# Kernel tuning notes

Measured on AMD Instinct MI355X. Metric: run time of the kernel, lower is better.

The kernel has to match this reference:

```python
import jax, jax.numpy as jnp
import numpy as np

B, IN_DIM, OUT_DIM, N, H = 64, 2, 1, 512, 64
SEQ, HOR, K, NSUP = 12, 12, 2, 2
TOT = 1 + NSUP * K  # number of diffusion matrices (identity + K steps per support)


def _lin_init(key, fan_in, shape):
    return jax.random.normal(key, shape, jnp.float32) / np.sqrt(fan_in)


def setup_inputs() -> dict:
    key = jax.random.key(0)
    ks = jax.random.split(key, 16)
    inputs = jax.random.normal(ks[0], (B, IN_DIM, N, SEQ), jnp.float32)
    A = jax.random.uniform(ks[1], (NSUP, N, N), jnp.float32)
    supports = A / A.sum(axis=2, keepdims=True)  # row-normalized transition matrices
    params = {}
    i = 2
    for pre, in0 in (('e', IN_DIM), ('d', OUT_DIM)):
        for l in range(2):
            cin = (in0 if l == 0 else H) + H
            params[f'{pre}{l}_wg'] = _lin_init(ks[i], TOT * cin, (TOT * cin, 2 * H)); i += 1
            params[f'{pre}{l}_bg'] = jnp.zeros((2 * H,), jnp.float32)
            params[f'{pre}{l}_wc'] = _lin_init(ks[i], TOT * cin, (TOT * cin, H)); i += 1
            params[f'{pre}{l}_bc'] = jnp.zeros((H,), jnp.float32)
    params['proj_w'] = _lin_init(ks[i], H, (OUT_DIM, H))
    params['proj_b'] = jnp.zeros((OUT_DIM,), jnp.float32)
    return {'inputs': inputs, 'supports': supports, **params}


def _gconv(x, h, supports, W, b):
    # x: (B,Cx,N), h: (B,H,N) -> (B,Dout,N)
    z = jnp.concatenate([x, h], axis=1)
    feats = [z]
    for s in range(NSUP):
        xk = z
        for _ in range(K):
            xk = jnp.einsum('nm,bcm->bcn', supports[s], xk)
            feats.append(xk)
    zf = jnp.concatenate(feats, axis=1)  # (B, TOT*C, N)
    return jnp.einsum('bcn,cd->bdn', zf, W) + b[None, :, None]


def _cell(x, h, supports, wg, bg, wc, bc):
    ru = jax.nn.sigmoid(_gconv(x, h, supports, wg, bg))
    r, u = jnp.split(ru, 2, axis=1)
    c = jnp.tanh(_gconv(x, r * h, supports, wc, bc))
    return u * h + (1.0 - u) * c


def _run(inputs, supports, p):
    h0 = jnp.zeros((B, H, N), jnp.float32)
    h1 = jnp.zeros((B, H, N), jnp.float32)

    def enc_step(carry, x):
        h0, h1 = carry
        h0 = _cell(x, h0, supports, p['e0_wg'], p['e0_bg'], p['e0_wc'], p['e0_bc'])
        h1 = _cell(h0, h1, supports, p['e1_wg'], p['e1_bg'], p['e1_wc'], p['e1_bc'])
        return (h0, h1), None

    xs = jnp.moveaxis(inputs, -1, 0)  # (SEQ,B,IN_DIM,N)
    (h0, h1), _ = jax.lax.scan(enc_step, (h0, h1), xs)

    go = jnp.zeros((B, OUT_DIM, N), jnp.float32)

    def dec_step(carry, _):
        x, h0, h1 = carry
        h0 = _cell(x, h0, supports, p['d0_wg'], p['d0_bg'], p['d0_wc'], p['d0_bc'])
        h1 = _cell(h0, h1, supports, p['d1_wg'], p['d1_bg'], p['d1_wc'], p['d1_bc'])
        y = jnp.einsum('bhn,oh->bon', h1, p['proj_w']) + p['proj_b'][None, :, None]
        return (y, h0, h1), y

    _, ys = jax.lax.scan(dec_step, (go, h0, h1), None, length=HOR)
    return jnp.moveaxis(ys, 0, -1)  # (B, OUT_DIM, N, HOR)


def reference(inputs, supports, e0_wg, e0_bg, e0_wc, e0_bc, e1_wg, e1_bg, e1_wc, e1_bc,
              d0_wg, d0_bg, d0_wc, d0_bc, d1_wg, d1_bg, d1_wc, d1_bc, proj_w, proj_b):
    p = dict(e0_wg=e0_wg, e0_bg=e0_bg, e0_wc=e0_wc, e0_bc=e0_bc,
             e1_wg=e1_wg, e1_bg=e1_bg, e1_wc=e1_wc, e1_bc=e1_bc,
             d0_wg=d0_wg, d0_bg=d0_bg, d0_wc=d0_wc, d0_bc=d0_bc,
             d1_wg=d1_wg, d1_bg=d1_bg, d1_wc=d1_wc, d1_bc=d1_bc,
             proj_w=proj_w, proj_b=proj_b)
    return _run(inputs, supports, p)
```

## Files before the change

### kernel.cpp

```cpp
#include <hip/hip_runtime.h>

#define B_ 64
#define N_ 512

typedef __attribute__((ext_vector_type(8))) short bf8_t;
typedef __attribute__((ext_vector_type(16))) float f16_t;
typedef __attribute__((ext_vector_type(4))) float f4v_t;

#define MFMA32(a, b, c) __builtin_amdgcn_mfma_f32_32x32x16_bf16(a, b, c, 0, 0, 0)

__device__ __forceinline__ ushort f2bf(float x) {
  union { float f; unsigned u; } v; v.f = x;
  unsigned r = v.u + 0x7FFFu + ((v.u >> 16) & 1u);
  return (ushort)(r >> 16);
}
__device__ __forceinline__ float bf2f(ushort h) {
  union { unsigned u; float f; } v; v.u = ((unsigned)h) << 16;
  return v.f;
}

__device__ __forceinline__ void gld16(const ushort* g, ushort* l) {
  __builtin_amdgcn_global_load_lds(
      (const __attribute__((address_space(1))) unsigned int*)(uintptr_t)g,
      (__attribute__((address_space(3))) unsigned int*)(uintptr_t)l,
      16, 0, 0);
}

__device__ __forceinline__ int xcd_logical(int nwg) {
  int lin = blockIdx.x + gridDim.x * (blockIdx.y + gridDim.y * blockIdx.z);
  return (lin & 7) * (nwg >> 3) + (lin >> 3);
}

__device__ __forceinline__ int swz32(int r) { return (r >> 1) & 3; }

template <int ROWS, int THREADS>
__device__ __forceinline__ void stage_tile2(const ushort* g, int lda, int k0,
                                            ushort* l, int tid) {
  constexpr int RT = (ROWS * 32) / (THREADS * 8);
#pragma unroll
  for (int q = 0; q < RT; ++q) {
    int e  = q * THREADS * 8 + tid * 8;
    int r  = e >> 5;
    int c8 = (e >> 3) & 3;
    int g8 = c8 ^ swz32(r);
    gld16(g + (size_t)r * lda + k0 + g8 * 8, l + e);
  }
}

__device__ __forceinline__ int crow32(int r, int hb) {
  return (r & 3) + 8 * (r >> 2) + 4 * hb;
}

__device__ __forceinline__ void core128(
    const ushort* Ah, const ushort* Al, int lda,
    const ushort* Bh, const ushort* Bl, int ldb,
    int K, ushort* lds, f16_t acc[2][2]) {
  constexpr int TILE = 128 * 32;
  constexpr int SSZ  = 4 * TILE;
  const int tid = threadIdx.x, lane = tid & 63, wave = tid >> 6;
  const int ar = lane & 31, hb = lane >> 5;
  const int wm = wave >> 1, wn = wave & 1;

  auto stage = [&](int buf, int k0) {
    ushort* lb = lds + buf * SSZ;
    stage_tile2<128, 256>(Ah, lda, k0, lb, tid);
    stage_tile2<128, 256>(Al, lda, k0, lb + TILE, tid);
    stage_tile2<128, 256>(Bh, ldb, k0, lb + 2 * TILE, tid);
    stage_tile2<128, 256>(Bl, ldb, k0, lb + 3 * TILE, tid);
  };

  const int nc = K >> 5;
  stage(0, 0);
  int buf = 0;
  for (int c = 0; c < nc; ++c) {
    __syncthreads();
    if (c + 1 < nc) stage(buf ^ 1, (c + 1) << 5);
    const ushort* lb = lds + buf * SSZ;
#pragma unroll
    for (int ks = 0; ks < 2; ++ks) {
      bf8_t ah[2], al[2], bh[2], bl[2];
#pragma unroll
      for (int i = 0; i < 2; ++i) {
        int r = wm * 64 + 32 * i + ar;
        int c8 = (ks * 2 + hb) ^ swz32(r);
        ah[i] = *(const bf8_t*)(lb + r * 32 + c8 * 8);
        al[i] = *(const bf8_t*)(lb + TILE + r * 32 + c8 * 8);
      }
#pragma unroll
      for (int j = 0; j < 2; ++j) {
        int r = wn * 64 + 32 * j + ar;
        int c8 = (ks * 2 + hb) ^ swz32(r);
        bh[j] = *(const bf8_t*)(lb + 2 * TILE + r * 32 + c8 * 8);
        bl[j] = *(const bf8_t*)(lb + 3 * TILE + r * 32 + c8 * 8);
      }
#pragma unroll
      for (int i = 0; i < 2; ++i)
#pragma unroll
        for (int j = 0; j < 2; ++j) {
          acc[i][j] = MFMA32(ah[i], bh[j], acc[i][j]);
          acc[i][j] = MFMA32(ah[i], bl[j], acc[i][j]);
          acc[i][j] = MFMA32(al[i], bh[j], acc[i][j]);
        }
    }
    buf ^= 1;
  }
}

__device__ __forceinline__ void core128_1(
    const ushort* Ah, int lda,
    const ushort* Bh, int ldb,
    int K, ushort* lds, f16_t acc[2][2]) {
  constexpr int TILE = 128 * 32;
  constexpr int SSZ  = 2 * TILE;
  const int tid = threadIdx.x, lane = tid & 63, wave = tid >> 6;
  const int ar = lane & 31, hb = lane >> 5;
  const int wm = wave >> 1, wn = wave & 1;

  auto stage = [&](int buf, int k0) {
    ushort* lb = lds + buf * SSZ;
    stage_tile2<128, 256>(Ah, lda, k0, lb, tid);
    stage_tile2<128, 256>(Bh, ldb, k0, lb + TILE, tid);
  };

  const int nc = K >> 5;
  stage(0, 0);
  int buf = 0;
  for (int c = 0; c < nc; ++c) {
    __syncthreads();
    if (c + 1 < nc) stage(buf ^ 1, (c + 1) << 5);
    const ushort* lb = lds + buf * SSZ;
#pragma unroll
    for (int ks = 0; ks < 2; ++ks) {
      bf8_t ah[2], bh[2];
#pragma unroll
      for (int i = 0; i < 2; ++i) {
        int r = wm * 64 + 32 * i + ar;
        int c8 = (ks * 2 + hb) ^ swz32(r);
        ah[i] = *(const bf8_t*)(lb + r * 32 + c8 * 8);
      }
#pragma unroll
      for (int j = 0; j < 2; ++j) {
        int r = wn * 64 + 32 * j + ar;
        int c8 = (ks * 2 + hb) ^ swz32(r);
        bh[j] = *(const bf8_t*)(lb + TILE + r * 32 + c8 * 8);
      }
#pragma unroll
      for (int i = 0; i < 2; ++i)
#pragma unroll
        for (int j = 0; j < 2; ++j)
          acc[i][j] = MFMA32(ah[i], bh[j], acc[i][j]);
    }
    buf ^= 1;
  }
}

__global__ __launch_bounds__(256) void stb_k(const float* __restrict__ S,
                                             ushort* __restrict__ Bcat,
                                             ushort* __restrict__ STb) {
  __shared__ float tile[16][17];
  int s = blockIdx.z;
  int n0 = blockIdx.y * 16, m0 = blockIdx.x * 16;
  int tx = threadIdx.x & 15, ty = threadIdx.x >> 4;
  float v = S[(size_t)s * 262144 + (size_t)(n0 + ty) * 512 + m0 + tx];
  tile[ty][tx] = v;
  Bcat[(size_t)(n0 + ty) * 2048 + (size_t)(2 * s) * 512 + m0 + tx] = f2bf(v);
  __syncthreads();
  STb[(size_t)s * 262144 + (size_t)(m0 + ty) * 512 + n0 + tx] = f2bf(tile[tx][ty]);
}

__global__ __launch_bounds__(256) void ssqm_k(const ushort* __restrict__ Bc,
                                              const ushort* __restrict__ STb,
                                              ushort* __restrict__ Bout) {
  __shared__ __attribute__((aligned(16))) ushort lds[2 * 2 * 128 * 32];
  int tid = threadIdx.x, lane = tid & 63, wave = tid >> 6;
  int wm = wave >> 1, wn = wave & 1, ar = lane & 31, hb = lane >> 5;
  int a = blockIdx.x, bm = blockIdx.y, s = blockIdx.z;
  f16_t acc[2][2] = {};
  core128_1(Bc + (size_t)(a * 128) * 2048 + (size_t)(2 * s) * 512, 2048,
            STb + (size_t)s * 262144 + (size_t)(bm * 128) * 512, 512,
            512, lds, acc);
#pragma unroll
  for (int i = 0; i < 2; ++i)
#pragma unroll
    for (int j = 0; j < 2; ++j) {
      int m_ = bm * 128 + wn * 64 + 32 * j + ar;
#pragma unroll
      for (int r = 0; r < 16; ++r) {
        int n_ = a * 128 + wm * 64 + 32 * i + crow32(r, hb);
        Bout[(size_t)n_ * 2048 + (size_t)(2 * s + 1) * 512 + m_] = f2bf(acc[i][j][r]);
      }
    }
}

struct WSrc { const float* wg[4]; const float* wc[4]; };

__global__ __launch_bounds__(256) void wprep_all_k(WSrc src,
                                                   ushort* __restrict__ Wbuf) {
  int idx = blockIdx.x * 256 + threadIdx.x;
  if (idx >= 4 * 147456) return;
  int ci = idx / 147456, r = idx % 147456;
  int C = (ci == 0) ? 66 : (ci == 2) ? 65 : 128;
  const float* WG = src.wg[ci];
  const float* WC = src.wc[ci];
  ushort v;
  if (r < 32768) {
    int e = r & 16383, c = e & 127, d = e >> 7;
    float x = (c < C) ? WG[(size_t)c * 128 + d] : 0.f;
    ushort hh = f2bf(x);
    v = (r < 16384) ? hh : f2bf(x - bf2f(hh));
  } else if (r < 98304) {
    int e = r - 32768, c = e & 127, i = e >> 7;
    int t = 1 + (i >> 7), d = i & 127;
    v = (c < C) ? f2bf(WG[(size_t)(t * C + c) * 128 + d]) : (ushort)0;
  } else if (r < 114688) {
    int e = (r - 98304) & 8191, c = e & 127, d = e >> 7;
    float x = (c < C) ? WC[(size_t)c * 64 + d] : 0.f;
    ushort hh = f2bf(x);
    v = (r < 106496) ? hh : f2bf(x - bf2f(hh));
  } else {
    int e = r - 114688, c = e & 127, i = e >> 7;
    int t = 1 + (i >> 6), d = i & 63;
    v = (c < C) ? f2bf(WC[(size_t)(t * C + c) * 64 + d]) : (ushort)0;
  }
  Wbuf[idx] = v;
}

__global__ __launch_bounds__(256) void packzT_k(const float* __restrict__ xsrc,
                                                int xmode, int t, int Cx, int C,
                                                const float* __restrict__ hT,
                                                ushort* __restrict__ Zh,
                                                ushort* __restrict__ Zl) {
  int jg = blockIdx.x * 256 + threadIdx.x;
  int b = jg >> 9, n = jg & 511;
  for (int c0 = 0; c0 < 128; c0 += 8) {
    bf8_t vh, vl;
#pragma unroll
    for (int q = 0; q < 8; ++q) {
      int c = c0 + q;
      float v;
      if (c < Cx) {
        if (xmode == 0)      v = xsrc[((size_t)(b * Cx + c) * 512 + n) * 12 + t];
        else if (xmode == 1) v = xsrc[jg];
        else                 v = xsrc[(size_t)jg * 64 + c];
      } else if (c < C) {
        v = hT[(size_t)jg * 64 + (c - Cx)];
      } else {
        v = 0.f;
      }
      ushort hh = f2bf(v);
      vh[q] = (short)hh;
      vl[q] = (short)f2bf(v - bf2f(hh));
    }
    *(bf8_t*)(Zh + (size_t)jg * 128 + c0) = vh;
    *(bf8_t*)(Zl + (size_t)jg * 128 + c0) = vl;
  }
}

template <int MODE>
__global__ __launch_bounds__(256, 2) void g1_k(const ushort* __restrict__ Wih,
                                               const ushort* __restrict__ Wil,
                                               const ushort* __restrict__ Wd,
                                               const ushort* __restrict__ Zh,
                                               const ushort* __restrict__ Zl,
                                               ushort* __restrict__ Gh,
                                               float* __restrict__ G0T, int K) {
  __shared__ __attribute__((aligned(16))) ushort lds[2 * 4 * 128 * 32];
  constexpr int DR = (MODE == 0) ? 128 : 64;
  constexpr int NMT = (MODE == 0) ? 4 : 2;
  int tid = threadIdx.x, lane = tid & 63, wave = tid >> 6;
  int wm = wave >> 1, wn = wave & 1, ar = lane & 31, hb = lane >> 5;
  int L = xcd_logical(256 * (NMT + 1));
  int mt = L % (NMT + 1), nt = L / (NMT + 1);
  f16_t acc[2][2] = {};
  if (mt == NMT) {
    core128(Wih, Wil, 128,
            Zh + (size_t)nt * 128 * 128, Zl + (size_t)nt * 128 * 128, 128,
            K, lds, acc);
#pragma unroll
    for (int i = 0; i < 2; ++i)
#pragma unroll
      for (int j = 0; j < 2; ++j) {
        int jg = nt * 128 + wn * 64 + 32 * j + ar;
#pragma unroll
        for (int r = 0; r < 16; ++r) {
          int d = wm * 64 + 32 * i + crow32(r, hb);
          if (d >= DR) continue;
          G0T[(size_t)jg * DR + d] = acc[i][j][r];
        }
      }
  } else {
    core128_1(Wd + (size_t)mt * 128 * 128, 128,
              Zh + (size_t)nt * 128 * 128, 128,
              K, lds, acc);
#pragma unroll
    for (int i = 0; i < 2; ++i)
#pragma unroll
      for (int j = 0; j < 2; ++j) {
        int jg = nt * 128 + wn * 64 + 32 * j + ar;
        int b = jg >> 9, m = jg & 511;
#pragma unroll
        for (int r = 0; r < 16; ++r) {
          int ii = mt * 128 + wm * 64 + 32 * i + crow32(r, hb);
          int tt = ii / DR, d = ii % DR;
          Gh[((size_t)(b * DR + d)) * 2048 + (size_t)tt * 512 + m] = f2bf(acc[i][j][r]);
        }
      }
  }
}

__global__ __launch_bounds__(256, 3) void ru1g_k(const ushort* __restrict__ Gh,
                                                 const ushort* __restrict__ Bch,
                                                 float* __restrict__ P) {
  __shared__ __attribute__((aligned(16))) ushort lds[2 * 2 * 128 * 32];
  int tid = threadIdx.x, lane = tid & 63, wave = tid >> 6;
  int wm = wave >> 1, wn = wave & 1, ar = lane & 31, hb = lane >> 5;
  int L = xcd_logical(768);
  int mt = L & 3, nt = (L >> 2) & 63, kz = L >> 8;
  int k0 = kz * 768;
  int K  = (kz == 2) ? 512 : 768;
  f16_t acc[2][2] = {};
  core128_1(Bch + (size_t)mt * 128 * 2048 + k0, 2048,
            Gh + (size_t)nt * 128 * 2048 + k0, 2048,
            K, lds, acc);
  float* Pz = P + (size_t)kz * 4194304;
#pragma unroll
  for (int i = 0; i < 2; ++i)
#pragma unroll
    for (int j = 0; j < 2; ++j) {
      int R = nt * 128 + wn * 64 + 32 * j + ar;
      int b = R >> 7, d = R & 127;
#pragma unroll
      for (int r = 0; r < 16; ++r) {
        int node = mt * 128 + wm * 64 + 32 * i + crow32(r, hb);
        Pz[((size_t)b * 512 + node) * 128 + d] = acc[i][j][r];
      }
    }
}

__global__ __launch_bounds__(256) void ru1f_k(const float* __restrict__ P,
                                              const float* __restrict__ G0T,
                                              const float* __restrict__ bg,
                                              const float* __restrict__ hT,
                                              float* __restrict__ U,
                                              ushort* __restrict__ Zh,
                                              ushort* __restrict__ Zl, int Cx) {
  int i4 = blockIdx.x * 256 + threadIdx.x;
  if (i4 >= 1048576) return;
  int base = i4 * 4;
  int row = base >> 7, d = base & 127;
  f4v_t p0 = *(const f4v_t*)(P + base);
  f4v_t p1 = *(const f4v_t*)(P + 4194304 + base);
  f4v_t p2 = *(const f4v_t*)(P + 2 * 4194304 + base);
  f4v_t g0 = *(const f4v_t*)(G0T + base);
  if (d < 64) {
    f4v_t hv = *(const f4v_t*)(hT + (size_t)row * 64 + d);
#pragma unroll
    for (int e = 0; e < 4; ++e) {
      float s = 1.f / (1.f + expf(-(p0[e] + p1[e] + p2[e] + g0[e] + bg[d + e])));
      float rh = s * hv[e];
      ushort hh = f2bf(rh);
      Zh[(size_t)row * 128 + Cx + d + e] = hh;
      Zl[(size_t)row * 128 + Cx + d + e] = f2bf(rh - bf2f(hh));
    }
  } else {
    f4v_t uo;
#pragma unroll
    for (int e = 0; e < 4; ++e)
      uo[e] = 1.f / (1.f + expf(-(p0[e] + p1[e] + p2[e] + g0[e] + bg[d + e])));
    *(f4v_t*)(U + (size_t)row * 64 + (d - 64)) = uo;
  }
}

__global__ __launch_bounds__(256, 3) void ru2g_k(const ushort* __restrict__ Gh,
                                                 const ushort* __restrict__ Bch,
                                                 float* __restrict__ P) {
  __shared__ __attribute__((aligned(16))) ushort lds[2 * 2 * 128 * 32];
  int tid = threadIdx.x, lane = tid & 63, wave = tid >> 6;
  int wm = wave >> 1, wn = wave & 1, ar = lane & 31, hb = lane >> 5;
  int L = xcd_logical(512);
  int mt = L & 3, nt = (L >> 2) & 31, kz = L >> 7;
  f16_t acc[2][2] = {};
  core128_1(Bch + (size_t)mt * 128 * 2048 + kz * 512, 2048,
            Gh + (size_t)nt * 128 * 2048 + kz * 512, 2048,
            512, lds, acc);
  float* Pz = P + (size_t)kz * 2097152;
#pragma unroll
  for (int i = 0; i < 2; ++i)
#pragma unroll
    for (int j = 0; j < 2; ++j) {
      int R = nt * 128 + wn * 64 + 32 * j + ar;
      int b = R >> 6, d = R & 63;
#pragma unroll
      for (int r = 0; r < 16; ++r) {
        int node = mt * 128 + wm * 64 + 32 * i + crow32(r, hb);
        Pz[((size_t)b * 512 + node) * 64 + d] = acc[i][j][r];
      }
    }
}

__global__ __launch_bounds__(256) void ru2f_k(const float* __restrict__ P,
                                              const float* __restrict__ G0c,
                                              const float* __restrict__ bc,
                                              const float* __restrict__ U,
                                              float* __restrict__ hT) {
  int i4 = blockIdx.x * 256 + threadIdx.x;
  if (i4 >= 524288) return;
  int base = i4 * 4;
  int d = base & 63;
  f4v_t p0 = *(const f4v_t*)(P + base);
  f4v_t p1 = *(const f4v_t*)(P + 2097152 + base);
  f4v_t p2 = *(const f4v_t*)(P + 2 * 2097152 + base);
  f4v_t p3 = *(const f4v_t*)(P + 3 * 2097152 + base);
  f4v_t g0 = *(const f4v_t*)(G0c + base);
  f4v_t uv = *(const f4v_t*)(U + base);
  f4v_t hv = *(const f4v_t*)(hT + base);
#pragma unroll
  for (int e = 0; e < 4; ++e) {
    float ct = tanhf(p0[e] + p1[e] + p2[e] + p3[e] + g0[e] + bc[d + e]);
    hv[e] = uv[e] * hv[e] + (1.f - uv[e]) * ct;
  }
  *(f4v_t*)(hT + base) = hv;
}

__global__ __launch_bounds__(256) void proj_out_k(const float* __restrict__ h1T,
                                                  const float* __restrict__ pw,
                                                  const float* __restrict__ pb,
                                                  float* __restrict__ ybuf,
                                                  float* __restrict__ out, int k) {
  int idx = blockIdx.x * blockDim.x + threadIdx.x;
  if (idx >= B_ * N_) return;
  float s = pb[0];
  const float* hrow = h1T + (size_t)idx * 64;
#pragma unroll
  for (int j = 0; j < 64; ++j)
    s = fmaf(pw[j], hrow[j], s);
  ybuf[idx] = s;
  out[(size_t)idx * 12 + k] = s;
}

extern "C" void kernel_launch(void* const* d_in, const int* in_sizes, int n_in,
                              void* d_out, int out_size, void* d_ws, size_t ws_size,
                              hipStream_t stream) {
  const float* inputs   = (const float*)d_in[0];
  const float* supports = (const float*)d_in[1];
  WSrc wsrc;
  wsrc.wg[0] = (const float*)d_in[2];  wsrc.wg[1] = (const float*)d_in[6];
  wsrc.wg[2] = (const float*)d_in[10]; wsrc.wg[3] = (const float*)d_in[14];
  wsrc.wc[0] = (const float*)d_in[4];  wsrc.wc[1] = (const float*)d_in[8];
  wsrc.wc[2] = (const float*)d_in[12]; wsrc.wc[3] = (const float*)d_in[16];
  const float* Bg[4] = { (const float*)d_in[3],  (const float*)d_in[7],
                         (const float*)d_in[11], (const float*)d_in[15] };
  const float* Bc[4] = { (const float*)d_in[5],  (const float*)d_in[9],
                         (const float*)d_in[13], (const float*)d_in[17] };
  const float* proj_w = (const float*)d_in[18];
  const float* proj_b = (const float*)d_in[19];
  float* out = (float*)d_out;

  char* p = (char*)d_ws;
  auto carve = [&](size_t bytes) { void* q = p; p += (bytes + 255) & ~(size_t)255; return q; };
  ushort* Bch  = (ushort*)carve((size_t)512 * 2048 * 2);
  ushort* zTh  = (ushort*)carve((size_t)32768 * 128 * 2);
  ushort* zTl  = (ushort*)carve((size_t)32768 * 128 * 2);
  ushort* Gh   = (ushort*)carve((size_t)8192 * 2048 * 2);
  float*  G0T  = (float*)carve((size_t)32768 * 128 * 4);
  float*  P    = (float*)carve((size_t)3 * 4194304 * 4);
  float*  U    = (float*)carve((size_t)2097152 * 4);
  float*  h0   = (float*)carve((size_t)2097152 * 4);
  float*  h1   = (float*)carve((size_t)2097152 * 4);
  float*  ybuf = (float*)carve((size_t)B_ * N_ * 4);
  ushort* Wbuf = (ushort*)carve((size_t)4 * 147456 * 2);
  ushort* STb  = (ushort*)U;

  hipMemsetAsync(h0, 0, (size_t)2097152 * 4 * 2 + (size_t)B_ * N_ * 4, stream);

  stb_k<<<dim3(32, 32, 2), 256, 0, stream>>>(supports, Bch, STb);
  ssqm_k<<<dim3(4, 4, 2), 256, 0, stream>>>(Bch, STb, Bch);
  wprep_all_k<<<(4 * 147456 + 255) / 256, 256, 0, stream>>>(wsrc, Wbuf);

  auto cell = [&](int ci, int Cx, const float* x, int xmode, int t, float* h) {
    int C = Cx + 64;
    int K1 = (C + 31) & ~31;
    ushort* cw = Wbuf + (size_t)ci * 147456;
    ushort* Wgid_h = cw;          ushort* Wgid_l = cw + 16384;
    ushort* Wgd    = cw + 32768;
    ushort* Wcid_h = cw + 98304;  ushort* Wcid_l = cw + 106496;
    ushort* Wcd    = cw + 114688;
    packzT_k<<<128, 256, 0, stream>>>(x, xmode, t, Cx, C, h, zTh, zTl);
    g1_k<0><<<dim3(256, 5), 256, 0, stream>>>(Wgid_h, Wgid_l, Wgd, zTh, zTl, Gh, G0T, K1);
    ru1g_k<<<dim3(64, 4, 3), 256, 0, stream>>>(Gh, Bch, P);
    ru1f_k<<<4096, 256, 0, stream>>>(P, G0T, Bg[ci], h, U, zTh, zTl, Cx);
    g1_k<1><<<dim3(256, 3), 256, 0, stream>>>(Wcid_h, Wcid_l, Wcd, zTh, zTl, Gh, G0T, K1);
    ru2g_k<<<dim3(32, 4, 4), 256, 0, stream>>>(Gh, Bch, P);
    ru2f_k<<<2048, 256, 0, stream>>>(P, G0T, Bc[ci], U, h);
  };

  for (int t = 0; t < 12; ++t) {
    cell(0, 2, inputs, 0, t, h0);
    cell(1, 64, h0, 2, 0, h1);
  }
  for (int k = 0; k < 12; ++k) {
    cell(2, 1, ybuf, 1, 0, h0);
    cell(3, 64, h0, 2, 0, h1);
    proj_out_k<<<(B_ * N_ + 255) / 256, 256, 0, stream>>>(h1, proj_w, proj_b, ybuf, out, k);
  }
}
```

Measured before the change: 6.229 ms.

## Fuse Z-buffer packing into epilogues and shrink layer-0 K to 96

Drops the per-cell packzT_k kernel. ru2f_k and proj_out_k now write the bf16 hi/lo split of the new hidden state straight into persistent per-layer Z buffers, so layer 1's input comes from layer 0's epilogue and the decoder feedback from the projection. Layer-0 cells get their own 96-wide Z buffer, so the first GEMM uses K=96 instead of 128. Only the raw inputs are still packed each encoder step, plus a one-time transpose at the encoder/decoder switch. The cost is extra scalar bf16 stores in the elementwise epilogues, and correctness now depends on the zero-initialised padding columns staying valid.

```diff
diff --git a/kernel.cpp b/kernel.cpp
--- a/kernel.cpp
+++ b/kernel.cpp
@@ -225,35 +225,30 @@
   Wbuf[idx] = v;
 }
 
-__global__ __launch_bounds__(256) void packzT_k(const float* __restrict__ xsrc,
-                                                int xmode, int t, int Cx, int C,
-                                                const float* __restrict__ hT,
-                                                ushort* __restrict__ Zh,
-                                                ushort* __restrict__ Zl) {
+__global__ __launch_bounds__(256) void packx_k(const float* __restrict__ xsrc,
+                                               int t, ushort* __restrict__ Zh,
+                                               ushort* __restrict__ Zl) {
   int jg = blockIdx.x * 256 + threadIdx.x;
   int b = jg >> 9, n = jg & 511;
-  for (int c0 = 0; c0 < 128; c0 += 8) {
-    bf8_t vh, vl;
-#pragma unroll
-    for (int q = 0; q < 8; ++q) {
-      int c = c0 + q;
-      float v;
-      if (c < Cx) {
-        if (xmode == 0)      v = xsrc[((size_t)(b * Cx + c) * 512 + n) * 12 + t];
-        else if (xmode == 1) v = xsrc[jg];
-        else                 v = xsrc[(size_t)jg * 64 + c];
-      } else if (c < C) {
-        v = hT[(size_t)jg * 64 + (c - Cx)];
-      } else {
-        v = 0.f;
-      }
-      ushort hh = f2bf(v);
-      vh[q] = (short)hh;
-      vl[q] = (short)f2bf(v - bf2f(hh));
-    }
-    *(bf8_t*)(Zh + (size_t)jg * 128 + c0) = vh;
-    *(bf8_t*)(Zl + (size_t)jg * 128 + c0) = vl;
-  }
+#pragma unroll
+  for (int c = 0; c < 2; ++c) {
+    float v = xsrc[((size_t)(b * 2 + c) * 512 + n) * 12 + t];
+    ushort hh = f2bf(v);
+    Zh[(size_t)jg * 96 + c] = hh;
+    Zl[(size_t)jg * 96 + c] = f2bf(v - bf2f(hh));
+  }
+}
+
+__global__ __launch_bounds__(256) void trans_k(const float* __restrict__ hT0,
+                                               ushort* __restrict__ Zh,
+                                               ushort* __restrict__ Zl) {
+  int idx = blockIdx.x * 256 + threadIdx.x;
+  if (idx >= 32768 * 96) return;
+  int col = idx % 96, row = idx / 96;
+  float v = (col >= 1 && col <= 64) ? hT0[(size_t)row * 64 + (col - 1)] : 0.f;
+  ushort hh = f2bf(v);
+  Zh[(size_t)row * 96 + col] = hh;
+  Zl[(size_t)row * 96 + col] = f2bf(v - bf2f(hh));
 }
 
 template <int MODE>
@@ -263,7 +258,8 @@
                                                const ushort* __restrict__ Zh,
                                                const ushort* __restrict__ Zl,
                                                ushort* __restrict__ Gh,
-                                               float* __restrict__ G0T, int K) {
+                                               float* __restrict__ G0T,
+                                               int K, int zs) {
   __shared__ __attribute__((aligned(16))) ushort lds[2 * 4 * 128 * 32];
   constexpr int DR = (MODE == 0) ? 128 : 64;
   constexpr int NMT = (MODE == 0) ? 4 : 2;
@@ -274,7 +270,7 @@
   f16_t acc[2][2] = {};
   if (mt == NMT) {
     core128(Wih, Wil, 128,
-            Zh + (size_t)nt * 128 * 128, Zl + (size_t)nt * 128 * 128, 128,
+            Zh + (size_t)nt * 128 * zs, Zl + (size_t)nt * 128 * zs, zs,
             K, lds, acc);
 #pragma unroll
     for (int i = 0; i < 2; ++i)
@@ -290,7 +286,7 @@
       }
   } else {
     core128_1(Wd + (size_t)mt * 128 * 128, 128,
-              Zh + (size_t)nt * 128 * 128, 128,
+              Zh + (size_t)nt * 128 * zs, zs,
               K, lds, acc);
 #pragma unroll
     for (int i = 0; i < 2; ++i)
@@ -343,7 +339,8 @@
                                               const float* __restrict__ hT,
                                               float* __restrict__ U,
                                               ushort* __restrict__ Zh,
-                                              ushort* __restrict__ Zl, int Cx) {
+                                              ushort* __restrict__ Zl,
+                                              int cx, int zs) {
   int i4 = blockIdx.x * 256 + threadIdx.x;
   if (i4 >= 1048576) return;
   int base = i4 * 4;
@@ -359,8 +356,8 @@
       float s = 1.f / (1.f + expf(-(p0[e] + p1[e] + p2[e] + g0[e] + bg[d + e])));
       float rh = s * hv[e];
       ushort hh = f2bf(rh);
-      Zh[(size_t)row * 128 + Cx + d + e] = hh;
-      Zl[(size_t)row * 128 + Cx + d + e] = f2bf(rh - bf2f(hh));
+      Zh[(size_t)row * zs + cx + d + e] = hh;
+      Zl[(size_t)row * zs + cx + d + e] = f2bf(rh - bf2f(hh));
     }
   } else {
     f4v_t uo;
@@ -402,11 +399,16 @@
                                               const float* __restrict__ G0c,
                                               const float* __restrict__ bc,
                                               const float* __restrict__ U,
-                                              float* __restrict__ hT) {
+                                              float* __restrict__ hT,
+                                              ushort* __restrict__ Zsh,
+                                              ushort* __restrict__ Zsl,
+                                              int sx, int zs,
+                                              ushort* __restrict__ Z1h,
+                                              ushort* __restrict__ Z1l) {
   int i4 = blockIdx.x * 256 + threadIdx.x;
   if (i4 >= 524288) return;
   int base = i4 * 4;
-  int d = base & 63;
+  int row = base >> 6, d = base & 63;
   f4v_t p0 = *(const f4v_t*)(P + base);
   f4v_t p1 = *(const f4v_t*)(P + 2097152 + base);
   f4v_t p2 = *(const f4v_t*)(P + 2 * 2097152 + base);
@@ -418,6 +420,14 @@
   for (int e = 0; e < 4; ++e) {
     float ct = tanhf(p0[e] + p1[e] + p2[e] + p3[e] + g0[e] + bc[d + e]);
     hv[e] = uv[e] * hv[e] + (1.f - uv[e]) * ct;
+    ushort hh = f2bf(hv[e]);
+    ushort ll = f2bf(hv[e] - bf2f(hh));
+    Zsh[(size_t)row * zs + sx + d + e] = hh;
+    Zsl[(size_t)row * zs + sx + d + e] = ll;
+    if (Z1h) {
+      Z1h[(size_t)row * 128 + d + e] = hh;
+      Z1l[(size_t)row * 128 + d + e] = ll;
+    }
   }
   *(f4v_t*)(hT + base) = hv;
 }
@@ -425,8 +435,9 @@
 __global__ __launch_bounds__(256) void proj_out_k(const float* __restrict__ h1T,
                                                   const float* __restrict__ pw,
                                                   const float* __restrict__ pb,
-                                                  float* __restrict__ ybuf,
-                                                  float* __restrict__ out, int k) {
+                                                  float* __restrict__ out, int k,
+                                                  ushort* __restrict__ Z0h,
+                                                  ushort* __restrict__ Z0l) {
   int idx = blockIdx.x * blockDim.x + threadIdx.x;
   if (idx >= B_ * N_) return;
   float s = pb[0];
@@ -434,8 +445,10 @@
 #pragma unroll
   for (int j = 0; j < 64; ++j)
     s = fmaf(pw[j], hrow[j], s);
-  ybuf[idx] = s;
   out[(size_t)idx * 12 + k] = s;
+  ushort hh = f2bf(s);
+  Z0h[(size_t)idx * 96] = hh;
+  Z0l[(size_t)idx * 96] = f2bf(s - bf2f(hh));
 }
 
 extern "C" void kernel_launch(void* const* d_in, const int* in_sizes, int n_in,
@@ -459,48 +472,58 @@
   char* p = (char*)d_ws;
   auto carve = [&](size_t bytes) { void* q = p; p += (bytes + 255) & ~(size_t)255; return q; };
   ushort* Bch  = (ushort*)carve((size_t)512 * 2048 * 2);
-  ushort* zTh  = (ushort*)carve((size_t)32768 * 128 * 2);
-  ushort* zTl  = (ushort*)carve((size_t)32768 * 128 * 2);
   ushort* Gh   = (ushort*)carve((size_t)8192 * 2048 * 2);
   float*  G0T  = (float*)carve((size_t)32768 * 128 * 4);
   float*  P    = (float*)carve((size_t)3 * 4194304 * 4);
-  float*  U    = (float*)carve((size_t)2097152 * 4);
+  ushort* Wbuf = (ushort*)carve((size_t)4 * 147456 * 2);
+  ushort* zT0h = (ushort*)carve((size_t)32768 * 96 * 2);
+  ushort* zT0l = (ushort*)carve((size_t)32768 * 96 * 2);
+  ushort* zT1h = (ushort*)carve((size_t)32768 * 128 * 2);
+  ushort* zT1l = (ushort*)carve((size_t)32768 * 128 * 2);
   float*  h0   = (float*)carve((size_t)2097152 * 4);
   float*  h1   = (float*)carve((size_t)2097152 * 4);
-  float*  ybuf = (float*)carve((size_t)B_ * N_ * 4);
-  ushort* Wbuf = (ushort*)carve((size_t)4 * 147456 * 2);
+  float*  U    = (float*)carve((size_t)2097152 * 4);
   ushort* STb  = (ushort*)U;
 
-  hipMemsetAsync(h0, 0, (size_t)2097152 * 4 * 2 + (size_t)B_ * N_ * 4, stream);
+  size_t zero_bytes = (size_t)32768 * 96 * 2 * 2 + (size_t)32768 * 128 * 2 * 2 +
+                      (size_t)2097152 * 4 * 2;
+  hipMemsetAsync(zT0h, 0, zero_bytes, stream);
 
   stb_k<<<dim3(32, 32, 2), 256, 0, stream>>>(supports, Bch, STb);
   ssqm_k<<<dim3(4, 4, 2), 256, 0, stream>>>(Bch, STb, Bch);
   wprep_all_k<<<(4 * 147456 + 255) / 256, 256, 0, stream>>>(wsrc, Wbuf);
 
-  auto cell = [&](int ci, int Cx, const float* x, int xmode, int t, float* h) {
-    int C = Cx + 64;
-    int K1 = (C + 31) & ~31;
+  auto cell = [&](int ci) {
     ushort* cw = Wbuf + (size_t)ci * 147456;
     ushort* Wgid_h = cw;          ushort* Wgid_l = cw + 16384;
     ushort* Wgd    = cw + 32768;
     ushort* Wcid_h = cw + 98304;  ushort* Wcid_l = cw + 106496;
     ushort* Wcd    = cw + 114688;
-    packzT_k<<<128, 256, 0, stream>>>(x, xmode, t, Cx, C, h, zTh, zTl);
-    g1_k<0><<<dim3(256, 5), 256, 0, stream>>>(Wgid_h, Wgid_l, Wgd, zTh, zTl, Gh, G0T, K1);
+    bool l0 = (ci == 0 || ci == 2);
+    ushort* Zh = l0 ? zT0h : zT1h;
+    ushort* Zl = l0 ? zT0l : zT1l;
+    int zs = l0 ? 96 : 128;
+    int K1 = l0 ? 96 : 128;
+    int cx = (ci == 0) ? 2 : (ci == 2) ? 1 : 64;
+    float* h = l0 ? h0 : h1;
+    g1_k<0><<<dim3(256, 5), 256, 0, stream>>>(Wgid_h, Wgid_l, Wgd, Zh, Zl, Gh, G0T, K1, zs);
     ru1g_k<<<dim3(64, 4, 3), 256, 0, stream>>>(Gh, Bch, P);
-    ru1f_k<<<4096, 256, 0, stream>>>(P, G0T, Bg[ci], h, U, zTh, zTl, Cx);
-    g1_k<1><<<dim3(256, 3), 256, 0, stream>>>(Wcid_h, Wcid_l, Wcd, zTh, zTl, Gh, G0T, K1);
+    ru1f_k<<<4096, 256, 0, stream>>>(P, G0T, Bg[ci], h, U, Zh, Zl, cx, zs);
+    g1_k<1><<<dim3(256, 3), 256, 0, stream>>>(Wcid_h, Wcid_l, Wcd, Zh, Zl, Gh, G0T, K1, zs);
     ru2g_k<<<dim3(32, 4, 4), 256, 0, stream>>>(Gh, Bch, P);
-    ru2f_k<<<2048, 256, 0, stream>>>(P, G0T, Bc[ci], U, h);
+    ru2f_k<<<2048, 256, 0, stream>>>(P, G0T, Bc[ci], U, h, Zh, Zl, cx, zs,
+                                     l0 ? zT1h : nullptr, l0 ? zT1l : nullptr);
   };
 
   for (int t = 0; t < 12; ++t) {
-    cell(0, 2, inputs, 0, t, h0);
-    cell(1, 64, h0, 2, 0, h1);
-  }
+    packx_k<<<128, 256, 0, stream>>>(inputs, t, zT0h, zT0l);
+    cell(0);
+    cell(1);
+  }
+  trans_k<<<(32768 * 96 + 255) / 256, 256, 0, stream>>>(h0, zT0h, zT0l);
   for (int k = 0; k < 12; ++k) {
-    cell(2, 1, ybuf, 1, 0, h0);
-    cell(3, 64, h0, 2, 0, h1);
-    proj_out_k<<<(B_ * N_ + 255) / 256, 256, 0, stream>>>(h1, proj_w, proj_b, ybuf, out, k);
-  }
-}
+    cell(2);
+    cell(3);
+    proj_out_k<<<128, 256, 0, stream>>>(h1, proj_w, proj_b, out, k, zT0h, zT0l);
+  }
+}
```

After: 5.294 ms. -15.0%, faster.
